# Optimization experiments

Measured on AMD Instinct MI355X. Metric: run time of the kernel, lower is better.

## Reference

```python
import jax, jax.numpy as jnp
import numpy as np

REDUCTION = 32
NUM_CLASSES = 20
COORD_SCALE = 1.0
NOOBJECT_SCALE = 1.0
OBJECT_SCALE = 5.0
CLASS_SCALE = 1.0
IOU_THRES = 0.6
ANCHORS = [[1.3221, 1.73145], [3.19275, 4.00944], [5.05587, 8.09892], [9.47112, 4.84053], [11.2364, 10.0071]]


def bbox_ious(boxes1, boxes2):
    # boxes in center format (cx, cy, w, h). boxes1 [..., N, 4], boxes2 [..., M, 4] -> [..., N, M]
    b1 = boxes1[..., :, None, :]
    b2 = boxes2[..., None, :, :]
    b1x1, b1y1 = b1[..., 0] - b1[..., 2] / 2, b1[..., 1] - b1[..., 3] / 2
    b1x2, b1y2 = b1[..., 0] + b1[..., 2] / 2, b1[..., 1] + b1[..., 3] / 2
    b2x1, b2y1 = b2[..., 0] - b2[..., 2] / 2, b2[..., 1] - b2[..., 3] / 2
    b2x2, b2y2 = b2[..., 0] + b2[..., 2] / 2, b2[..., 1] + b2[..., 3] / 2
    dx = jnp.clip(jnp.minimum(b1x2, b2x2) - jnp.maximum(b1x1, b2x1), 0.0)
    dy = jnp.clip(jnp.minimum(b1y2, b2y2) - jnp.maximum(b1y1, b2y1), 0.0)
    inter = dx * dy
    union = (b1x2 - b1x1) * (b1y2 - b1y1) + (b2x2 - b2x1) * (b2y2 - b2y1) - inter
    return inter / union


def setup_inputs() -> dict:
    key = jax.random.key(0)
    k1, k2, k3, k4, k5 = jax.random.split(key, 5)
    B, H, W, A, C, G = 16, 64, 64, 5, NUM_CLASSES, 32
    output = jax.random.normal(k1, (B, A * (5 + C), H, W), jnp.float32) * 0.5
    img = W * REDUCTION  # 2048 px image
    wh = jax.random.uniform(k2, (B, G, 2), jnp.float32, 4.0, 200.0)  # box w,h in pixels
    xy = jax.random.uniform(k3, (B, G, 2), jnp.float32, 0.0, 1.0) * (img - wh)  # top-left corner
    cls = jax.random.randint(k4, (B, G, 1), 0, C).astype(jnp.float32)
    target = jnp.concatenate([xy, wh, cls], axis=-1)  # [B, G, 5] = (x, y, w, h, class)
    gt_valid = jax.random.uniform(k5, (B, G)) < 0.75
    anchors = jnp.array(ANCHORS, jnp.float32)
    return {"output": output, "target": target, "gt_valid": gt_valid, "anchors": anchors}


def reference(output, target, gt_valid, anchors):
    B, _, H, W = output.shape
    A = anchors.shape[0]
    C = NUM_CLASSES
    HW = H * W
    out = output.reshape(B, A, 5 + C, HW)
    coord = jnp.concatenate([jax.nn.sigmoid(out[:, :, :2]), out[:, :, 2:4]], axis=2)  # [B,A,4,HW]
    conf = jax.nn.sigmoid(out[:, :, 4])  # [B,A,HW]
    cls_logits = jnp.transpose(out[:, :, 5:], (0, 1, 3, 2)).reshape(-1, C)  # [B*A*HW, C]

    # ---- decoded (detached) prediction boxes in grid units ----
    lin_x = jnp.tile(jnp.arange(W, dtype=output.dtype), H)      # hw % W
    lin_y = jnp.repeat(jnp.arange(H, dtype=output.dtype), W)    # hw // W
    cd = jax.lax.stop_gradient(coord)
    px = cd[:, :, 0] + lin_x
    py = cd[:, :, 1] + lin_y
    pw = jnp.exp(cd[:, :, 2]) * anchors[:, 0][None, :, None]
    ph = jnp.exp(cd[:, :, 3]) * anchors[:, 1][None, :, None]
    pred_boxes = jnp.stack([px, py, pw, ph], axis=-1).reshape(B, A * HW, 4)

    # ---- build_targets, fully vectorized ----
    tgt = jax.lax.stop_gradient(target)
    gx = (tgt[..., 0] + tgt[..., 2] / 2) / REDUCTION
    gy = (tgt[..., 1] + tgt[..., 3] / 2) / REDUCTION
    gw = tgt[..., 2] / REDUCTION
    gh = tgt[..., 3] / REDUCTION
    gt = jnp.stack([gx, gy, gw, gh], axis=-1)  # [B,G,4]
    valid = gt_valid  # [B,G]

    iou_gt_pred = bbox_ious(gt, pred_boxes)  # [B,G,A*HW]
    ignore = jnp.any((iou_gt_pred > IOU_THRES) & valid[:, :, None], axis=1)  # [B,A*HW]
    conf_mask = jnp.where(ignore, 0.0, NOOBJECT_SCALE).astype(output.dtype)  # [B,A*HW]

    gt_wh = gt.at[..., :2].set(0.0)
    anchors_wh = jnp.concatenate([jnp.zeros_like(anchors), anchors], axis=1)  # [A,4]
    best_n = jnp.argmax(bbox_ious(gt_wh, anchors_wh), axis=-1)  # [B,G]

    gi = jnp.clip(gx.astype(jnp.int32), 0, W - 1)
    gj = jnp.clip(gy.astype(jnp.int32), 0, H - 1)
    cell = gj * W + gi  # [B,G]
    iou_best = jnp.take_along_axis(iou_gt_pred, (best_n * HW + cell)[..., None], axis=-1)[..., 0]  # [B,G]

    N = B * A * HW
    bidx = jnp.arange(B)[:, None]
    flat = jnp.where(valid, bidx * (A * HW) + best_n * HW + cell, N).reshape(-1)  # invalid -> OOB, dropped
    aw = anchors[best_n, 0]
    ah = anchors[best_n, 1]
    tc = jnp.stack([gx - gi, gy - gj,
                    jnp.log(jnp.maximum(gw, 1.0) / aw),
                    jnp.log(jnp.maximum(gh, 1.0) / ah)], axis=-1).reshape(-1, 4)

    coord_mask = jnp.zeros((N,), output.dtype).at[flat].set(1.0, mode='drop')
    cls_mask = jnp.zeros((N,), bool).at[flat].set(True, mode='drop')
    conf_mask = conf_mask.reshape(-1).at[flat].set(OBJECT_SCALE, mode='drop')
    tcoord = jnp.zeros((N, 4), output.dtype).at[flat].set(tc, mode='drop')
    tconf = jnp.zeros((N,), output.dtype).at[flat].set(iou_best.reshape(-1), mode='drop')
    tcls = jnp.zeros((N,), jnp.int32).at[flat].set(tgt[..., 4].astype(jnp.int32).reshape(-1), mode='drop')

    # ---- losses (sum reductions, / batch_size) ----
    coord_mask4 = coord_mask.reshape(B, A, 1, HW)
    tcoord4 = jnp.transpose(tcoord.reshape(B, A, HW, 4), (0, 1, 3, 2))  # [B,A,4,HW]
    conf_mask_s = jnp.sqrt(conf_mask.reshape(B, A, HW))
    loss_coord = COORD_SCALE * jnp.sum(((coord - tcoord4) * coord_mask4) ** 2) / B
    loss_conf = jnp.sum(((conf - tconf.reshape(B, A, HW)) * conf_mask_s) ** 2) / B
    logp = jax.nn.log_softmax(cls_logits, axis=-1)
    ce = -jnp.take_along_axis(logp, tcls[:, None], axis=-1)[:, 0]
    loss_cls = CLASS_SCALE * 2.0 * jnp.sum(jnp.where(cls_mask, ce, 0.0)) / B
    return loss_coord + loss_conf + loss_cls
```

## Files before the change

### kernel.cpp

```cpp
#include <hip/hip_runtime.h>
#include <math.h>

#define NB   16
#define NA   5
#define NC   20
#define NG   32
#define HWSZ 4096
#define WDIM 64
#define NCH  25
#define OBJ_SCALE 5.0f
#define NBLK ((NB * NA * HWSZ) / 256)

__global__ __launch_bounds__(256) void yolo_loss(
    const float* __restrict__ output,
    const float* __restrict__ target,
    const void*  __restrict__ gt_valid_raw,
    const float* __restrict__ anchors,
    float* __restrict__ partials,
    float* __restrict__ out)
{
    __shared__ float4 sbox[NG];
    __shared__ float2 sthr[NG];
    __shared__ float  sga [NG];
    __shared__ float  stx [NG], sty[NG], stw[NG], sth2[NG], scls[NG];
    __shared__ float  wsum[4];

    int tid  = threadIdx.x;
    int idx  = blockIdx.x * 256 + tid;
    int b    = idx / (NA * HWSZ);
    int rem  = idx % (NA * HWSZ);
    int a    = rem / HWSZ;
    int cell = rem % HWSZ;

    if (tid < 64) {
        const unsigned char* bytes = (const unsigned char*)gt_valid_raw;
        unsigned char bb = bytes[tid] | bytes[tid + 64] | bytes[tid + 128] | bytes[tid + 192];
        unsigned long long m = __ballot(bb != 0);
        bool is_u8  = (m & 0x2222222222222222ULL) != 0ULL;
        bool is_f32 = !is_u8 && (m & 0xCCCCCCCCCCCCCCCCULL) != 0ULL;

        if (tid < NG) {
            int t = b * NG + tid;
            bool valid;
            if (is_u8)       valid = bytes[t] != 0;
            else if (is_f32) valid = ((const float*)gt_valid_raw)[t] != 0.0f;
            else             valid = ((const int*)gt_valid_raw)[t]   != 0;

            const float* tg = target + t * 5;
            float x = tg[0], y = tg[1], w = tg[2], h = tg[3], cls = tg[4];
            const float inv = 1.0f / 32.0f;
            float gx = (x + 0.5f * w) * inv;
            float gy = (y + 0.5f * h) * inv;
            float gw = w * inv, gh = h * inv;
            float garea = gw * gh;

            int best = 0; float bi = -1.0f, baw = 1.0f, bah = 1.0f;
            #pragma unroll
            for (int n = 0; n < NA; ++n) {
                float aw_ = anchors[2*n], ah_ = anchors[2*n + 1];
                float inter = fminf(gw, aw_) * fminf(gh, ah_);
                float iou   = inter / (garea + aw_ * ah_ - inter);
                if (iou > bi) { bi = iou; best = n; baw = aw_; bah = ah_; }
            }
            int gi = min(max((int)gx, 0), WDIM - 1);
            int gj = min(max((int)gy, 0), WDIM - 1);

            if (valid) {
                sbox[tid] = make_float4(gx - 0.5f*gw, gy - 0.5f*gh,
                                        gx + 0.5f*gw, gy + 0.5f*gh);
                sthr[tid] = make_float2(0.375f * garea,
                                        (best == a) ? (float)(gj * WDIM + gi) : -1.0f);
            } else {
                sbox[tid] = make_float4(1e30f, 1e30f, -1e30f, -1e30f);
                sthr[tid] = make_float2(0.0f, -1.0f);
            }
            sga [tid] = garea;
            stx [tid] = gx - (float)gi;
            sty [tid] = gy - (float)gj;
            stw [tid] = logf(fmaxf(gw, 1.0f) / baw);
            sth2[tid] = logf(fmaxf(gh, 1.0f) / bah);
            scls[tid] = cls;
        }
    }
    __syncthreads();

    const float* base = output + ((size_t)(b * NA + a) * NCH) * HWSZ + cell;
    float ox = base[0];
    float oy = base[1 * HWSZ];
    float ow = base[2 * HWSZ];
    float oh = base[3 * HWSZ];
    float oc = base[4 * HWSZ];

    float sx   = 1.0f / (1.0f + __expf(-ox));
    float sy   = 1.0f / (1.0f + __expf(-oy));
    float conf = 1.0f / (1.0f + __expf(-oc));
    float pw = __expf(ow) * anchors[2 * a];
    float ph = __expf(oh) * anchors[2 * a + 1];
    float px = sx + (float)(cell & (WDIM - 1));
    float py = sy + (float)(cell >> 6);
    float px1 = px - 0.5f * pw, px2 = px + 0.5f * pw;
    float py1 = py - 0.5f * ph, py2 = py + 0.5f * ph;
    float parea = pw * ph;

    float negc1 = -0.375f * parea;
    float cellf = (float)cell;
    bool  ignore = false;
    int   match  = -1;
    #pragma unroll
    for (int g = 0; g < NG; ++g) {
        float4 bx = sbox[g];
        float2 tc = sthr[g];
        float dx = fminf(px2, bx.z) - fmaxf(px1, bx.x);
        float dy = fminf(py2, bx.w) - fmaxf(py1, bx.y);
        dx = fmaxf(dx, 0.0f); dy = fmaxf(dy, 0.0f);
        ignore |= (fmaf(dx, dy, negc1) > tc.x);
        if (tc.y == cellf) match = g;
    }

    float lsum  = 0.0f;
    float cm    = ignore ? 0.0f : 1.0f;
    float tconf = 0.0f;
    if (match >= 0) {
        cm = OBJ_SCALE;
        float4 bx = sbox[match];
        float dx = fmaxf(fminf(px2, bx.z) - fmaxf(px1, bx.x), 0.0f);
        float dy = fmaxf(fminf(py2, bx.w) - fmaxf(py1, bx.y), 0.0f);
        float inter = dx * dy;
        tconf = inter / (parea + sga[match] - inter);
        float d0 = sx - stx [match];
        float d1 = sy - sty [match];
        float d2 = ow - stw [match];
        float d3 = oh - sth2[match];
        lsum += d0*d0 + d1*d1 + d2*d2 + d3*d3;
        int tcl = (int)scls[match];
        float lg[NC];
        float m = -1e30f, ltgt = 0.0f;
        #pragma unroll
        for (int c = 0; c < NC; ++c) {
            lg[c] = base[(5 + c) * HWSZ];
            m = fmaxf(m, lg[c]);
            if (c == tcl) ltgt = lg[c];
        }
        float se = 0.0f;
        #pragma unroll
        for (int c = 0; c < NC; ++c) se += __expf(lg[c] - m);
        float ce = -(ltgt - m - __logf(se));
        lsum += 2.0f * ce;
    }
    float dc = conf - tconf;
    lsum += cm * dc * dc;

    #pragma unroll
    for (int off = 32; off > 0; off >>= 1) lsum += __shfl_down(lsum, off);
    int lane = tid & 63, wid = tid >> 6;
    if (lane == 0) wsum[wid] = lsum;
    __syncthreads();
    if (tid == 0) {
        float bs = wsum[0] + wsum[1] + wsum[2] + wsum[3];
        if (partials) partials[blockIdx.x] = bs;
        else          atomicAdd(out, bs * (1.0f / 16.0f));
    }
}

__global__ __launch_bounds__(256) void yolo_reduce(const float* __restrict__ partials,
                                                   float* __restrict__ out)
{
    int tid = threadIdx.x;
    float s = 0.0f;
    #pragma unroll
    for (int i = 0; i < NBLK / 256; ++i) s += partials[i * 256 + tid];
    #pragma unroll
    for (int off = 32; off > 0; off >>= 1) s += __shfl_down(s, off);
    __shared__ float wsum[4];
    int lane = tid & 63, wid = tid >> 6;
    if (lane == 0) wsum[wid] = s;
    __syncthreads();
    if (tid == 0) out[0] = (wsum[0] + wsum[1] + wsum[2] + wsum[3]) * (1.0f / 16.0f);
}

extern "C" void kernel_launch(void* const* d_in, const int* in_sizes, int n_in,
                              void* d_out, int out_size, void* d_ws, size_t ws_size,
                              hipStream_t stream) {
    const float* output   = (const float*)d_in[0];
    const float* target   = (const float*)d_in[1];
    const void*  gt_valid = d_in[2];
    const float* anchors  = (const float*)d_in[3];
    float* out = (float*)d_out;

    if (ws_size >= NBLK * sizeof(float)) {
        float* partials = (float*)d_ws;
        yolo_loss<<<NBLK, 256, 0, stream>>>(output, target, gt_valid, anchors, partials, out);
        yolo_reduce<<<1, 256, 0, stream>>>(partials, out);
    } else {
        hipMemsetAsync(out, 0, sizeof(float), stream);
        yolo_loss<<<NBLK, 256, 0, stream>>>(output, target, gt_valid, anchors, nullptr, out);
    }
}
```

Measured before the change: 15.60 us.

## Fuse final reduction into main kernel via per-block flags and last-block wait

Removes the second reduce kernel launch. Each block publishes its partial with a release flag, and the last block spins on every flag, sums the partials and resets the flags for the next call. This saves one launch, but assumes the flags start at zero and relies on the last-indexed block spinning while the other blocks finish. The fallback path for a small workspace now always uses two kernels, one of them lacking the atomic path.

New measurement: 22.39 us. 43.6% more time.

```diff
diff --git a/kernel.cpp b/kernel.cpp
--- a/kernel.cpp
+++ b/kernel.cpp
@@ -11,19 +11,17 @@
 #define OBJ_SCALE 5.0f
 #define NBLK ((NB * NA * HWSZ) / 256)
 
-__global__ __launch_bounds__(256) void yolo_loss(
+__device__ __forceinline__ float yolo_block_partial(
     const float* __restrict__ output,
     const float* __restrict__ target,
     const void*  __restrict__ gt_valid_raw,
     const float* __restrict__ anchors,
-    float* __restrict__ partials,
-    float* __restrict__ out)
+    float* wsum )
 {
     __shared__ float4 sbox[NG];
     __shared__ float2 sthr[NG];
     __shared__ float  sga [NG];
     __shared__ float  stx [NG], sty[NG], stw[NG], sth2[NG], scls[NG];
-    __shared__ float  wsum[4];
 
     int tid  = threadIdx.x;
     int idx  = blockIdx.x * 256 + tid;
@@ -155,11 +153,60 @@
     int lane = tid & 63, wid = tid >> 6;
     if (lane == 0) wsum[wid] = lsum;
     __syncthreads();
+    return wsum[0] + wsum[1] + wsum[2] + wsum[3];
+}
+
+__global__ __launch_bounds__(256, 5) void yolo_loss_fused(
+    const float* __restrict__ output,
+    const float* __restrict__ target,
+    const void*  __restrict__ gt_valid_raw,
+    const float* __restrict__ anchors,
+    float* __restrict__ partials,
+    unsigned int* __restrict__ flags,
+    float* __restrict__ out)
+{
+    __shared__ float wsum[4];
+    float bs = yolo_block_partial(output, target, gt_valid_raw, anchors, wsum);
+
+    int tid = threadIdx.x;
     if (tid == 0) {
-        float bs = wsum[0] + wsum[1] + wsum[2] + wsum[3];
-        if (partials) partials[blockIdx.x] = bs;
-        else          atomicAdd(out, bs * (1.0f / 16.0f));
-    }
+        __hip_atomic_store(&partials[blockIdx.x], bs,
+                           __ATOMIC_RELAXED, __HIP_MEMORY_SCOPE_AGENT);
+        __hip_atomic_store(&flags[blockIdx.x], 1u,
+                           __ATOMIC_RELEASE, __HIP_MEMORY_SCOPE_AGENT);
+    }
+
+    if (blockIdx.x != NBLK - 1) return;
+
+    float s = 0.0f;
+    #pragma unroll
+    for (int k = 0; k < NBLK / 256; ++k) {
+        int i = k * 256 + tid;
+        while (__hip_atomic_load(&flags[i], __ATOMIC_ACQUIRE,
+                                 __HIP_MEMORY_SCOPE_AGENT) != 1u) {
+            __builtin_amdgcn_s_sleep(2);
+        }
+        s += __hip_atomic_load(&partials[i], __ATOMIC_RELAXED,
+                               __HIP_MEMORY_SCOPE_AGENT);
+        __hip_atomic_store(&flags[i], 0u, __ATOMIC_RELAXED,
+                           __HIP_MEMORY_SCOPE_AGENT);
+    }
+    #pragma unroll
+    for (int off = 32; off > 0; off >>= 1) s += __shfl_down(s, off);
+    int lane = tid & 63, wid = tid >> 6;
+    if (lane == 0) wsum[wid] = s;
+    __syncthreads();
+    if (tid == 0) out[0] = (wsum[0] + wsum[1] + wsum[2] + wsum[3]) * (1.0f / 16.0f);
+}
+
+__global__ __launch_bounds__(256) void yolo_loss2(
+    const float* __restrict__ output, const float* __restrict__ target,
+    const void*  __restrict__ gt_valid_raw, const float* __restrict__ anchors,
+    float* __restrict__ partials)
+{
+    __shared__ float wsum[4];
+    float bs = yolo_block_partial(output, target, gt_valid_raw, anchors, wsum);
+    if (threadIdx.x == 0) partials[blockIdx.x] = bs;
 }
 
 __global__ __launch_bounds__(256) void yolo_reduce(const float* __restrict__ partials,
@@ -187,12 +234,14 @@
     const float* anchors  = (const float*)d_in[3];
     float* out = (float*)d_out;
 
-    if (ws_size >= NBLK * sizeof(float)) {
+    if (ws_size >= NBLK * (sizeof(float) + sizeof(unsigned int))) {
+        float*        partials = (float*)d_ws;
+        unsigned int* flags    = (unsigned int*)((char*)d_ws + NBLK * sizeof(float));
+        yolo_loss_fused<<<NBLK, 256, 0, stream>>>(output, target, gt_valid, anchors,
+                                                  partials, flags, out);
+    } else {
         float* partials = (float*)d_ws;
-        yolo_loss<<<NBLK, 256, 0, stream>>>(output, target, gt_valid, anchors, partials, out);
+        yolo_loss2<<<NBLK, 256, 0, stream>>>(output, target, gt_valid, anchors, partials);
         yolo_reduce<<<1, 256, 0, stream>>>(partials, out);
-    } else {
-        hipMemsetAsync(out, 0, sizeof(float), stream);
-        yolo_loss<<<NBLK, 256, 0, stream>>>(output, target, gt_valid, anchors, nullptr, out);
-    }
-}
+    }
+}
```
